# Kernel tuning notes

Hardware: AMD Instinct MI355X
Metric: run time of the kernel (lower is better)

## Reference

```python
import jax, jax.numpy as jnp
import numpy as np

N, E, F_IN, HID, K, CLS = 50000, 800000, 512, 128, 4, 40
EPS = 0.3


def setup_inputs() -> dict:
    key = jax.random.key(0)
    ks = jax.random.split(key, 6)
    x = jax.random.normal(ks[0], (N, F_IN), dtype=jnp.float32)
    edge_index = jax.random.randint(ks[1], (2, E), 0, N, dtype=jnp.int32)
    # xavier_normal with gain=1.414 ~ gain*sqrt(2/(fan_in+fan_out))
    t1_w = jax.random.normal(ks[2], (HID, F_IN), jnp.float32) * (1.414 * np.sqrt(2.0 / (F_IN + HID)))
    t1_b = jnp.zeros((HID,), jnp.float32)
    gate_w = jax.random.normal(ks[3], (K, 2 * HID), jnp.float32) * (1.414 * np.sqrt(2.0 / (2 * HID + 1)))
    gate_b = jnp.zeros((K,), jnp.float32)
    t2_w = jax.random.normal(ks[4], (CLS, HID), jnp.float32) * (1.414 * np.sqrt(2.0 / (HID + CLS)))
    t2_b = jnp.zeros((CLS,), jnp.float32)
    return dict(x=x, edge_index=edge_index, t1_w=t1_w, t1_b=t1_b,
                gate_w=gate_w, gate_b=gate_b, t2_w=t2_w, t2_b=t2_b)


def _fa_layer(h, row, col, nd, gw, gb):
    # gate(cat[h_row, h_col]) as two matvecs (equivalent to concat + Linear)
    d = h.shape[1]
    g = jnp.tanh(h[row] @ gw[:d] + h[col] @ gw[d:] + gb)   # [E]
    norm = g * nd[row] * nd[col]                           # [E]
    msg = norm[:, None] * h[row]                           # x_j = h[source], [E, HID]
    # aggregate (add) into target nodes
    return jax.ops.segment_sum(msg, col, num_segments=h.shape[0])


def reference(x, edge_index, t1_w, t1_b, gate_w, gate_b, t2_w, t2_b):
    row, col = edge_index[0], edge_index[1]
    deg = jax.ops.segment_sum(jnp.ones((E,), x.dtype), row, num_segments=N)
    nd = jnp.clip(deg, 1.0, None) ** -0.5                  # degree^{-1/2}, clamped at 1
    h = jax.nn.relu(x @ t1_w.T + t1_b)                     # [N, HID]
    raw = h
    for k in range(K):
        h = EPS * raw + _fa_layer(h, row, col, nd, gate_w[k], gate_b[k])
    return jax.nn.log_softmax(h @ t2_w.T + t2_b, axis=1)   # [N, CLS]
```

## Files before the change

kernel.cpp:

```cpp
#include <hip/hip_runtime.h>
#include <math.h>

#define N_NODES 50000
#define N_EDGES 800000
#define F_IN    512
#define HID     128
#define K_LAYERS 4
#define N_CLS   40
#define EPS_C   0.3f
#define CAP     64

#define GB_BLOCKS 782
#define PB_BLOCKS 1563

typedef __bf16 bf16x8 __attribute__((ext_vector_type(8)));
typedef float  f32x4  __attribute__((ext_vector_type(4)));
typedef float  f32x2  __attribute__((ext_vector_type(2)));

__device__ inline unsigned short bfb(float f) {
    __bf16 b = (__bf16)f;
    return __builtin_bit_cast(unsigned short, b);
}
__device__ inline unsigned pack2(float a, float b) {
    return (unsigned)bfb(a) | ((unsigned)bfb(b) << 16);
}
__device__ inline float lo2(unsigned v) { return __builtin_bit_cast(float, v << 16); }
__device__ inline float hi2(unsigned v) { return __builtin_bit_cast(float, v & 0xffff0000u); }
__device__ inline bf16x8 ld_frag(const unsigned short* p) {
    uint4 q = *(const uint4*)p;
    return __builtin_bit_cast(bf16x8, q);
}
__device__ inline void acc_fp8(float g, uint2 v, float* acc) {
    f32x2 p0 = __builtin_amdgcn_cvt_pk_f32_fp8((int)v.x, false);
    f32x2 p1 = __builtin_amdgcn_cvt_pk_f32_fp8((int)v.x, true);
    f32x2 p2 = __builtin_amdgcn_cvt_pk_f32_fp8((int)v.y, false);
    f32x2 p3 = __builtin_amdgcn_cvt_pk_f32_fp8((int)v.y, true);
    acc[0] = fmaf(g, p0[0], acc[0]); acc[1] = fmaf(g, p0[1], acc[1]);
    acc[2] = fmaf(g, p1[0], acc[2]); acc[3] = fmaf(g, p1[1], acc[3]);
    acc[4] = fmaf(g, p2[0], acc[4]); acc[5] = fmaf(g, p2[1], acc[5]);
    acc[6] = fmaf(g, p3[0], acc[6]); acc[7] = fmaf(g, p3[1], acc[7]);
}

__global__ __launch_bounds__(256) void k_prep(const int* __restrict__ row,
                                              const int* __restrict__ col,
                                              int* __restrict__ deg,
                                              int* __restrict__ cur,
                                              int* __restrict__ bucket) {
    int e0 = (blockIdx.x * 256 + threadIdx.x) * 2;
    if (e0 >= N_EDGES) return;
    int2 r2 = *(const int2*)&row[e0];
    int2 c2 = *(const int2*)&col[e0];
    atomicAdd(&deg[r2.x], 1);
    atomicAdd(&deg[r2.y], 1);
    int p0 = atomicAdd(&cur[c2.x], 1);
    int p1 = atomicAdd(&cur[c2.y], 1);
    if (p0 < CAP) bucket[((size_t)c2.x << 6) + p0] = r2.x;
    if (p1 < CAP) bucket[((size_t)c2.y << 6) + p1] = r2.y;
}

#define GS 72
__global__ __launch_bounds__(256) void k_gemm(const float* __restrict__ x,
                                              const float* __restrict__ w,
                                              const float* __restrict__ bias,
                                              const float* __restrict__ gw,
                                              const int* __restrict__ deg,
                                              unsigned* __restrict__ h0b,
                                              unsigned short* __restrict__ h08,
                                              float2* __restrict__ pn0,
                                              float* __restrict__ bn0) {
    __shared__ __attribute__((aligned(16))) unsigned short As[64 * GS];
    __shared__ __attribute__((aligned(16))) unsigned short Bs[128 * GS];
    __shared__ float redA[64];
    __shared__ float redB[64];
    const int t    = threadIdx.x;
    const int lane = t & 63;
    const int wv   = t >> 6;
    const int wrow = wv >> 1;
    const int wcol = wv & 1;
    const int nb0  = blockIdx.x * 64;
    const int m16  = lane & 15;
    const int quad = lane >> 4;

    if (t < 64) { redA[t] = 0.f; redB[t] = 0.f; }

    f32x4 acc[2][4];
#pragma unroll
    for (int mi = 0; mi < 2; mi++)
#pragma unroll
        for (int ni = 0; ni < 4; ni++) acc[mi][ni] = (f32x4){0.f, 0.f, 0.f, 0.f};

    for (int k0 = 0; k0 < F_IN; k0 += 64) {
        __syncthreads();
        {
            int r  = t & 63;
            int kh = (t >> 6) * 16;
            int n  = nb0 + r;
            unsigned short* pl = &As[r * GS + kh];
            if (n < N_NODES) {
                const float* px = &x[(size_t)n * F_IN + k0 + kh];
#pragma unroll
                for (int q = 0; q < 2; q++) {
                    float4 f0 = *(const float4*)(px + q * 8);
                    float4 f1 = *(const float4*)(px + q * 8 + 4);
                    *(ushort4*)(pl + q * 8)     = make_ushort4(bfb(f0.x), bfb(f0.y), bfb(f0.z), bfb(f0.w));
                    *(ushort4*)(pl + q * 8 + 4) = make_ushort4(bfb(f1.x), bfb(f1.y), bfb(f1.z), bfb(f1.w));
                }
            } else {
#pragma unroll
                for (int q = 0; q < 4; q++) *(ushort4*)(pl + q * 4) = make_ushort4(0, 0, 0, 0);
            }
        }
        {
            int j  = t & 127;
            int kh = (t >> 7) * 32;
            const float* pw = &w[(size_t)j * F_IN + k0 + kh];
            unsigned short* pl = &Bs[j * GS + kh];
#pragma unroll
            for (int q = 0; q < 4; q++) {
                float4 f0 = *(const float4*)(pw + q * 8);
                float4 f1 = *(const float4*)(pw + q * 8 + 4);
                *(ushort4*)(pl + q * 8)     = make_ushort4(bfb(f0.x), bfb(f0.y), bfb(f0.z), bfb(f0.w));
                *(ushort4*)(pl + q * 8 + 4) = make_ushort4(bfb(f1.x), bfb(f1.y), bfb(f1.z), bfb(f1.w));
            }
        }
        __syncthreads();
#pragma unroll
        for (int kk = 0; kk < 64; kk += 32) {
            bf16x8 af[2], bfr[4];
#pragma unroll
            for (int mi = 0; mi < 2; mi++)
                af[mi] = ld_frag(&As[(wrow * 32 + mi * 16 + m16) * GS + kk + quad * 8]);
#pragma unroll
            for (int ni = 0; ni < 4; ni++)
                bfr[ni] = ld_frag(&Bs[(wcol * 64 + ni * 16 + m16) * GS + kk + quad * 8]);
#pragma unroll
            for (int mi = 0; mi < 2; mi++)
#pragma unroll
                for (int ni = 0; ni < 4; ni++)
                    acc[mi][ni] = __builtin_amdgcn_mfma_f32_16x16x32_bf16(af[mi], bfr[ni], acc[mi][ni], 0, 0, 0);
        }
    }
    float bj[4], ga[4], gb2[4];
#pragma unroll
    for (int ni = 0; ni < 4; ni++) {
        int f = wcol * 64 + ni * 16 + m16;
        bj[ni]  = bias[f];
        ga[ni]  = gw[f];
        gb2[ni] = gw[128 + f];
    }
    unsigned short* h0u = (unsigned short*)h0b;
    unsigned char*  h8u = (unsigned char*)h08;
#pragma unroll
    for (int mi = 0; mi < 2; mi++)
#pragma unroll
        for (int reg = 0; reg < 4; reg++) {
            int loc = wrow * 32 + mi * 16 + quad * 4 + reg;
            int n   = nb0 + loc;
            float pa = 0.f, pb = 0.f;
            if (n < N_NODES) {
#pragma unroll
                for (int ni = 0; ni < 4; ni++) {
                    float v = fmaxf(acc[mi][ni][reg] + bj[ni], 0.f);
                    int f = wcol * 64 + ni * 16 + m16;
                    h0u[(size_t)n * HID + f] = bfb(v);
                    int pk = __builtin_amdgcn_cvt_pk_fp8_f32(v, v, 0, false);
                    h8u[(size_t)n * HID + f] = (unsigned char)(pk & 0xff);
                    pa = fmaf(v, ga[ni], pa);
                    pb = fmaf(v, gb2[ni], pb);
                }
            }
#pragma unroll
            for (int d = 1; d <= 8; d <<= 1) {
                pa += __shfl_xor(pa, d);
                pb += __shfl_xor(pb, d);
            }
            if (m16 == 0) {
                atomicAdd(&redA[loc], pa);
                atomicAdd(&redB[loc], pb);
            }
        }
    __syncthreads();
    if (t < 64) {
        int n = nb0 + t;
        if (n < N_NODES) {
            float dv = fmaxf((float)deg[n], 1.0f);
            pn0[n] = make_float2(redA[t], 1.0f / sqrtf(dv));
            bn0[n] = redB[t];
        }
    }
}

#define ISSUE_GRP(BASE, A, B, C, D)                                  \
    {                                                                \
        int ea = __shfl(idx, (BASE) + esub);                         \
        int eb = __shfl(idx, (BASE) + esub + 4);                     \
        int ec = __shfl(idx, (BASE) + esub + 8);                     \
        int ed = __shfl(idx, (BASE) + esub + 12);                    \
        A = h8v[(size_t)ea * 16 + fg];                               \
        B = h8v[(size_t)eb * 16 + fg];                               \
        C = h8v[(size_t)ec * 16 + fg];                               \
        D = h8v[(size_t)ed * 16 + fg];                               \
    }

__global__ __launch_bounds__(256) void k_agg7(const unsigned short* __restrict__ h8,
                                              const unsigned* __restrict__ h0b,
                                              const float2* __restrict__ pn,
                                              const float* __restrict__ bn,
                                              const int* __restrict__ bucket,
                                              const int* __restrict__ cur,
                                              const float* __restrict__ gb_all, int k,
                                              unsigned short* __restrict__ out8,
                                              unsigned* __restrict__ out16,
                                              const float* __restrict__ gwn,
                                              float2* __restrict__ pnn,
                                              float* __restrict__ bnn) {
    const int node = blockIdx.x * 4 + (threadIdx.x >> 6);
    const int lane = threadIdx.x & 63;
    if (node >= N_NODES) return;
    const int esub = lane >> 4;
    const int fg   = lane & 15;

    const int    cntr = cur[node];
    int          idx  = bucket[((size_t)node << 6) + lane];
    const float2 pno  = pn[node];
    const float  bwr  = bn[node];
    uint4 h0v = ((const uint4*)h0b)[(size_t)node * 16 + fg];

    const int   cnt = min(cntr, CAP);
    if (lane >= cnt) idx = 0;
    const float ndc = pno.y;
    const float bw  = bwr + gb_all[k];

    const uint2* h8v = (const uint2*)h8;
    uint2 v0 = make_uint2(0, 0), v1 = v0, v2 = v0, v3 = v0;
    uint2 w0 = v0, w1 = v0, w2 = v0, w3 = v0;
    if (cnt > 0)  ISSUE_GRP(0,  v0, v1, v2, v3);
    if (cnt > 16) ISSUE_GRP(16, w0, w1, w2, w3);

    float g = 0.f;
    if (lane < cnt) {
        float2 pr = pn[idx];
        float tt = pr.x + bw;
        float ex = __expf(tt + tt);
        g = (1.f - 2.f / (ex + 1.f)) * pr.y * ndc;
    }

    float acc[8];
#pragma unroll
    for (int j = 0; j < 8; j++) acc[j] = 0.f;

    for (int base = 0; base < cnt; base += 16) {
        float g0 = __shfl(g, base + esub);
        float g1 = __shfl(g, base + esub + 4);
        float g2 = __shfl(g, base + esub + 8);
        float g3 = __shfl(g, base + esub + 12);
        uint2 c0 = v0, c1 = v1, c2 = v2, c3 = v3;
        v0 = w0; v1 = w1; v2 = w2; v3 = w3;
        if (base + 32 < cnt) ISSUE_GRP(base + 32, w0, w1, w2, w3);
        acc_fp8(g0, c0, acc);
        acc_fp8(g1, c1, acc);
        acc_fp8(g2, c2, acc);
        acc_fp8(g3, c3, acc);
    }

#pragma unroll
    for (int j = 0; j < 8; j++) {
        acc[j] += __shfl_xor(acc[j], 16);
        acc[j] += __shfl_xor(acc[j], 32);
    }

    float of[8];
    of[0] = fmaf(EPS_C, lo2(h0v.x), acc[0]); of[1] = fmaf(EPS_C, hi2(h0v.x), acc[1]);
    of[2] = fmaf(EPS_C, lo2(h0v.y), acc[2]); of[3] = fmaf(EPS_C, hi2(h0v.y), acc[3]);
    of[4] = fmaf(EPS_C, lo2(h0v.z), acc[4]); of[5] = fmaf(EPS_C, hi2(h0v.z), acc[5]);
    of[6] = fmaf(EPS_C, lo2(h0v.w), acc[6]); of[7] = fmaf(EPS_C, hi2(h0v.w), acc[7]);
    if (esub == 0) {
        if (gwn) {
            int p0 = __builtin_amdgcn_cvt_pk_fp8_f32(of[0], of[1], 0, false);
            p0     = __builtin_amdgcn_cvt_pk_fp8_f32(of[2], of[3], p0, true);
            int p1 = __builtin_amdgcn_cvt_pk_fp8_f32(of[4], of[5], 0, false);
            p1     = __builtin_amdgcn_cvt_pk_fp8_f32(of[6], of[7], p1, true);
            ((uint2*)out8)[(size_t)node * 16 + fg] = make_uint2((unsigned)p0, (unsigned)p1);
        } else {
            uint4 ov;
            ov.x = pack2(of[0], of[1]); ov.y = pack2(of[2], of[3]);
            ov.z = pack2(of[4], of[5]); ov.w = pack2(of[6], of[7]);
            ((uint4*)out16)[(size_t)node * 16 + fg] = ov;
        }
    }

    if (gwn) {
        const float4* gw4 = (const float4*)gwn;
        float4 wa0 = gw4[fg * 2], wa1 = gw4[fg * 2 + 1];
        float4 wb0 = gw4[32 + fg * 2], wb1 = gw4[32 + fg * 2 + 1];
        float pa = of[0] * wa0.x + of[1] * wa0.y + of[2] * wa0.z + of[3] * wa0.w
                 + of[4] * wa1.x + of[5] * wa1.y + of[6] * wa1.z + of[7] * wa1.w;
        float pb = of[0] * wb0.x + of[1] * wb0.y + of[2] * wb0.z + of[3] * wb0.w
                 + of[4] * wb1.x + of[5] * wb1.y + of[6] * wb1.z + of[7] * wb1.w;
#pragma unroll
        for (int d = 1; d <= 8; d <<= 1) {
            pa += __shfl_xor(pa, d);
            pb += __shfl_xor(pb, d);
        }
        if (lane == 0) { pnn[node] = make_float2(pa, ndc); bnn[node] = pb; }
    }
}

#define OB_BLOCKS 3125
__global__ __launch_bounds__(256) void k_out(const unsigned* __restrict__ hb,
                                             const float* __restrict__ w2,
                                             const float* __restrict__ b2,
                                             float* __restrict__ out) {
    __shared__ float ws[N_CLS][HID + 1];
    __shared__ float hs[4][HID];
    __shared__ float bs[N_CLS];
    const int t = threadIdx.x;
    for (int i = t; i < N_CLS * HID; i += 256) {
        ws[i / HID][i % HID] = w2[i];
    }
    if (t < N_CLS) bs[t] = b2[t];
    __syncthreads();
    const int wv = t >> 6, lane = t & 63;
#pragma unroll
    for (int it = 0; it < 4; it++) {
        const int node = blockIdx.x * 16 + wv * 4 + it;
        unsigned v = hb[((size_t)node << 6) + lane];
        hs[wv][2 * lane]     = lo2(v);
        hs[wv][2 * lane + 1] = hi2(v);
        float z = -INFINITY;
        if (lane < N_CLS) {
            float s = bs[lane];
#pragma unroll 8
            for (int kk = 0; kk < HID; kk++) s = fmaf(hs[wv][kk], ws[lane][kk], s);
            z = s;
        }
        float mx = z;
#pragma unroll
        for (int d = 32; d > 0; d >>= 1) mx = fmaxf(mx, __shfl_xor(mx, d));
        float ex = (z == -INFINITY) ? 0.f : expf(z - mx);
        float sum = ex;
#pragma unroll
        for (int d = 32; d > 0; d >>= 1) sum += __shfl_xor(sum, d);
        if (lane < N_CLS)
            out[(size_t)node * N_CLS + lane] = z - mx - logf(sum);
    }
}

extern "C" void kernel_launch(void* const* d_in, const int* in_sizes, int n_in,
                              void* d_out, int out_size, void* d_ws, size_t ws_size,
                              hipStream_t stream) {
    const float* x   = (const float*)d_in[0];
    const int*   ei  = (const int*)d_in[1];
    const float* t1w = (const float*)d_in[2];
    const float* t1b = (const float*)d_in[3];
    const float* gw  = (const float*)d_in[4];
    const float* gb  = (const float*)d_in[5];
    const float* t2w = (const float*)d_in[6];
    const float* t2b = (const float*)d_in[7];
    float* out = (float*)d_out;

    const int* row = ei;
    const int* col = ei + N_EDGES;

    char* p = (char*)d_ws;
    auto alloc = [&](size_t bytes) -> char* {
        char* q = p;
        p += (bytes + 255) & ~(size_t)255;
        return q;
    };
    unsigned*       h0b  = (unsigned*)alloc(sizeof(unsigned) * (size_t)N_NODES * 64);
    unsigned*       hF   = (unsigned*)alloc(sizeof(unsigned) * (size_t)N_NODES * 64);
    unsigned short* h08  = (unsigned short*)alloc(sizeof(unsigned short) * (size_t)N_NODES * 64);
    unsigned short* hA8  = (unsigned short*)alloc(sizeof(unsigned short) * (size_t)N_NODES * 64);
    unsigned short* hB8  = (unsigned short*)alloc(sizeof(unsigned short) * (size_t)N_NODES * 64);
    float2*         pn0  = (float2*)alloc(sizeof(float2) * N_NODES);
    float2*         pn1  = (float2*)alloc(sizeof(float2) * N_NODES);
    float*          bn0  = (float*)alloc(sizeof(float) * N_NODES);
    float*          bn1  = (float*)alloc(sizeof(float) * N_NODES);
    int*            degi = (int*)alloc(sizeof(int) * N_NODES);
    int*            cur  = (int*)alloc(sizeof(int) * N_NODES);
    int*            bucket = (int*)alloc(sizeof(int) * (size_t)N_NODES * CAP);

    hipMemsetAsync(degi, 0, sizeof(int) * N_NODES, stream);
    hipMemsetAsync(cur,  0, sizeof(int) * N_NODES, stream);

    const int wb = (N_NODES + 3) / 4;

    k_prep<<<PB_BLOCKS, 256, 0, stream>>>(row, col, degi, cur, bucket);
    k_gemm<<<GB_BLOCKS, 256, 0, stream>>>(x, t1w, t1b, gw, degi, h0b, h08, pn0, bn0);

    const unsigned short* hc8 = h08;
    unsigned short* ring8[2] = {hA8, hB8};
    const float2* pc = pn0;  float2* pnx = pn1;
    const float*  bc = bn0;  float*  bnx = bn1;
    for (int k = 0; k < K_LAYERS; k++) {
        const float* gwn = (k + 1 < K_LAYERS) ? (gw + (size_t)(k + 1) * 2 * HID) : nullptr;
        unsigned short* hn8 = ring8[k & 1];
        k_agg7<<<wb, 256, 0, stream>>>(hc8, h0b, pc, bc, bucket, cur, gb, k,
                                       hn8, hF, gwn, pnx, bnx);
        hc8 = hn8;
        const float2* tp = pc; pc = pnx; pnx = (float2*)tp;
        const float*  tb = bc; bc = bnx; bnx = (float*)tb;
    }

    k_out<<<OB_BLOCKS, 256, 0, stream>>>(hF, t2w, t2b, out);
}
```

Before: 462.5 us.

## Split features into two planes and aggregate in two phases per layer

Node features are stored as two 64-column planes, and each aggregation layer runs as two launches, one per plane. This halves the random-gather working set each launch touches, so it has a better chance of staying cache-resident. The edge gate is computed once in the first phase and stored in a per-edge buffer for the second phase. The prep kernel is fused into the GEMM launch, the GEMM tile grows to 128 rows, and nontemporal loads and stores are used. The cost is twice the aggregation launches, extra gate-buffer traffic, and a read-modify-write of the next layer's projections.

```diff
diff --git a/kernel.cpp b/kernel.cpp
--- a/kernel.cpp
+++ b/kernel.cpp
@@ -10,12 +10,15 @@
 #define EPS_C   0.3f
 #define CAP     64
 
-#define GB_BLOCKS 782
+#define GB_BLOCKS 391
 #define PB_BLOCKS 1563
+#define PS0 ((size_t)N_NODES * 64)
 
 typedef __bf16 bf16x8 __attribute__((ext_vector_type(8)));
 typedef float  f32x4  __attribute__((ext_vector_type(4)));
 typedef float  f32x2  __attribute__((ext_vector_type(2)));
+typedef unsigned u32x2 __attribute__((ext_vector_type(2)));
+typedef unsigned u32x4 __attribute__((ext_vector_type(4)));
 
 __device__ inline unsigned short bfb(float f) {
     __bf16 b = (__bf16)f;
@@ -41,65 +44,67 @@
     acc[6] = fmaf(g, p3[0], acc[6]); acc[7] = fmaf(g, p3[1], acc[7]);
 }
 
-__global__ __launch_bounds__(256) void k_prep(const int* __restrict__ row,
-                                              const int* __restrict__ col,
-                                              int* __restrict__ deg,
-                                              int* __restrict__ cur,
-                                              int* __restrict__ bucket) {
-    int e0 = (blockIdx.x * 256 + threadIdx.x) * 2;
-    if (e0 >= N_EDGES) return;
-    int2 r2 = *(const int2*)&row[e0];
-    int2 c2 = *(const int2*)&col[e0];
-    atomicAdd(&deg[r2.x], 1);
-    atomicAdd(&deg[r2.y], 1);
-    int p0 = atomicAdd(&cur[c2.x], 1);
-    int p1 = atomicAdd(&cur[c2.y], 1);
-    if (p0 < CAP) bucket[((size_t)c2.x << 6) + p0] = r2.x;
-    if (p1 < CAP) bucket[((size_t)c2.y << 6) + p1] = r2.y;
-}
-
 #define GS 72
-__global__ __launch_bounds__(256) void k_gemm(const float* __restrict__ x,
-                                              const float* __restrict__ w,
-                                              const float* __restrict__ bias,
-                                              const float* __restrict__ gw,
-                                              const int* __restrict__ deg,
-                                              unsigned* __restrict__ h0b,
-                                              unsigned short* __restrict__ h08,
-                                              float2* __restrict__ pn0,
-                                              float* __restrict__ bn0) {
-    __shared__ __attribute__((aligned(16))) unsigned short As[64 * GS];
+__global__ __launch_bounds__(256) void k_gemm_prep(const float* __restrict__ x,
+                                                   const float* __restrict__ w,
+                                                   const float* __restrict__ bias,
+                                                   const float* __restrict__ gw,
+                                                   const int* __restrict__ row,
+                                                   const int* __restrict__ col,
+                                                   int* __restrict__ deg,
+                                                   int* __restrict__ cur,
+                                                   int* __restrict__ bucket,
+                                                   unsigned short* __restrict__ h0,
+                                                   unsigned char* __restrict__ h8,
+                                                   float2* __restrict__ pn0,
+                                                   float* __restrict__ bn0) {
+    if (blockIdx.x >= GB_BLOCKS) {
+        int e0 = (blockIdx.x - GB_BLOCKS) * 512 + threadIdx.x * 2;
+        if (e0 < N_EDGES) {
+            int2 r2 = *(const int2*)&row[e0];
+            int2 c2 = *(const int2*)&col[e0];
+            atomicAdd(&deg[r2.x], 1);
+            atomicAdd(&deg[r2.y], 1);
+            int p0 = atomicAdd(&cur[c2.x], 1);
+            int p1 = atomicAdd(&cur[c2.y], 1);
+            if (p0 < CAP) bucket[((size_t)c2.x << 6) + p0] = r2.x;
+            if (p1 < CAP) bucket[((size_t)c2.y << 6) + p1] = r2.y;
+        }
+        return;
+    }
+
+    __shared__ __attribute__((aligned(16))) unsigned short As[128 * GS];
     __shared__ __attribute__((aligned(16))) unsigned short Bs[128 * GS];
-    __shared__ float redA[64];
-    __shared__ float redB[64];
+    __shared__ float redA[128];
+    __shared__ float redB[128];
     const int t    = threadIdx.x;
     const int lane = t & 63;
     const int wv   = t >> 6;
     const int wrow = wv >> 1;
     const int wcol = wv & 1;
-    const int nb0  = blockIdx.x * 64;
+    const int nb0  = blockIdx.x * 128;
     const int m16  = lane & 15;
     const int quad = lane >> 4;
 
-    if (t < 64) { redA[t] = 0.f; redB[t] = 0.f; }
-
-    f32x4 acc[2][4];
-#pragma unroll
-    for (int mi = 0; mi < 2; mi++)
+    if (t < 128) { redA[t] = 0.f; redB[t] = 0.f; }
+
+    f32x4 acc[4][4];
+#pragma unroll
+    for (int mi = 0; mi < 4; mi++)
 #pragma unroll
         for (int ni = 0; ni < 4; ni++) acc[mi][ni] = (f32x4){0.f, 0.f, 0.f, 0.f};
 
     for (int k0 = 0; k0 < F_IN; k0 += 64) {
         __syncthreads();
         {
-            int r  = t & 63;
-            int kh = (t >> 6) * 16;
+            int r  = t & 127;
+            int kh = (t >> 7) * 32;
             int n  = nb0 + r;
             unsigned short* pl = &As[r * GS + kh];
             if (n < N_NODES) {
                 const float* px = &x[(size_t)n * F_IN + k0 + kh];
 #pragma unroll
-                for (int q = 0; q < 2; q++) {
+                for (int q = 0; q < 4; q++) {
                     float4 f0 = *(const float4*)(px + q * 8);
                     float4 f1 = *(const float4*)(px + q * 8 + 4);
                     *(ushort4*)(pl + q * 8)     = make_ushort4(bfb(f0.x), bfb(f0.y), bfb(f0.z), bfb(f0.w));
@@ -107,7 +112,7 @@
                 }
             } else {
 #pragma unroll
-                for (int q = 0; q < 4; q++) *(ushort4*)(pl + q * 4) = make_ushort4(0, 0, 0, 0);
+                for (int q = 0; q < 8; q++) *(ushort4*)(pl + q * 4) = make_ushort4(0, 0, 0, 0);
             }
         }
         {
@@ -126,15 +131,15 @@
         __syncthreads();
 #pragma unroll
         for (int kk = 0; kk < 64; kk += 32) {
-            bf16x8 af[2], bfr[4];
-#pragma unroll
-            for (int mi = 0; mi < 2; mi++)
-                af[mi] = ld_frag(&As[(wrow * 32 + mi * 16 + m16) * GS + kk + quad * 8]);
+            bf16x8 af[4], bfr[4];
+#pragma unroll
+            for (int mi = 0; mi < 4; mi++)
+                af[mi] = ld_frag(&As[(wrow * 64 + mi * 16 + m16) * GS + kk + quad * 8]);
 #pragma unroll
             for (int ni = 0; ni < 4; ni++)
                 bfr[ni] = ld_frag(&Bs[(wcol * 64 + ni * 16 + m16) * GS + kk + quad * 8]);
 #pragma unroll
-            for (int mi = 0; mi < 2; mi++)
+            for (int mi = 0; mi < 4; mi++)
 #pragma unroll
                 for (int ni = 0; ni < 4; ni++)
                     acc[mi][ni] = __builtin_amdgcn_mfma_f32_16x16x32_bf16(af[mi], bfr[ni], acc[mi][ni], 0, 0, 0);
@@ -148,23 +153,23 @@
         ga[ni]  = gw[f];
         gb2[ni] = gw[128 + f];
     }
-    unsigned short* h0u = (unsigned short*)h0b;
-    unsigned char*  h8u = (unsigned char*)h08;
-#pragma unroll
-    for (int mi = 0; mi < 2; mi++)
+    unsigned short* h0pl = h0 + (size_t)wcol * PS0;
+    unsigned char*  h8pl = h8 + (size_t)wcol * PS0;
+#pragma unroll
+    for (int mi = 0; mi < 4; mi++)
 #pragma unroll
         for (int reg = 0; reg < 4; reg++) {
-            int loc = wrow * 32 + mi * 16 + quad * 4 + reg;
+            int loc = wrow * 64 + mi * 16 + quad * 4 + reg;
             int n   = nb0 + loc;
             float pa = 0.f, pb = 0.f;
             if (n < N_NODES) {
 #pragma unroll
                 for (int ni = 0; ni < 4; ni++) {
                     float v = fmaxf(acc[mi][ni][reg] + bj[ni], 0.f);
-                    int f = wcol * 64 + ni * 16 + m16;
-                    h0u[(size_t)n * HID + f] = bfb(v);
+                    int f16 = ni * 16 + m16;
+                    h0pl[(size_t)n * 64 + f16] = bfb(v);
                     int pk = __builtin_amdgcn_cvt_pk_fp8_f32(v, v, 0, false);
-                    h8u[(size_t)n * HID + f] = (unsigned char)(pk & 0xff);
+                    h8pl[(size_t)n * 64 + f16] = (unsigned char)(pk & 0xff);
                     pa = fmaf(v, ga[ni], pa);
                     pb = fmaf(v, gb2[ni], pb);
                 }
@@ -180,134 +185,139 @@
             }
         }
     __syncthreads();
-    if (t < 64) {
+    if (t < 128) {
         int n = nb0 + t;
         if (n < N_NODES) {
-            float dv = fmaxf((float)deg[n], 1.0f);
-            pn0[n] = make_float2(redA[t], 1.0f / sqrtf(dv));
+            ((float*)pn0)[2 * (size_t)n] = redA[t];
             bn0[n] = redB[t];
         }
     }
 }
 
-#define ISSUE_GRP(BASE, A, B, C, D)                                  \
-    {                                                                \
-        int ea = __shfl(idx, (BASE) + esub);                         \
-        int eb = __shfl(idx, (BASE) + esub + 4);                     \
-        int ec = __shfl(idx, (BASE) + esub + 8);                     \
-        int ed = __shfl(idx, (BASE) + esub + 12);                    \
-        A = h8v[(size_t)ea * 16 + fg];                               \
-        B = h8v[(size_t)eb * 16 + fg];                               \
-        C = h8v[(size_t)ec * 16 + fg];                               \
-        D = h8v[(size_t)ed * 16 + fg];                               \
-    }
-
-__global__ __launch_bounds__(256) void k_agg7(const unsigned short* __restrict__ h8,
-                                              const unsigned* __restrict__ h0b,
+__global__ __launch_bounds__(256) void k_nd(const int* __restrict__ deg,
+                                            float2* __restrict__ pn0) {
+    int n = blockIdx.x * 256 + threadIdx.x;
+    if (n < N_NODES) {
+        float dv = fmaxf((float)deg[n], 1.0f);
+        ((float*)pn0)[2 * (size_t)n + 1] = 1.0f / sqrtf(dv);
+    }
+}
+
+__global__ __launch_bounds__(256) void k_aggp(const unsigned char* __restrict__ h8p,
+                                              const unsigned short* __restrict__ h0p,
                                               const float2* __restrict__ pn,
                                               const float* __restrict__ bn,
                                               const int* __restrict__ bucket,
                                               const int* __restrict__ cur,
-                                              const float* __restrict__ gb_all, int k,
-                                              unsigned short* __restrict__ out8,
-                                              unsigned* __restrict__ out16,
+                                              const float* __restrict__ gb_all, int k, int phase,
+                                              float* __restrict__ garr,
+                                              unsigned char* __restrict__ out8p,
+                                              unsigned short* __restrict__ out16p,
                                               const float* __restrict__ gwn,
                                               float2* __restrict__ pnn,
                                               float* __restrict__ bnn) {
     const int node = blockIdx.x * 4 + (threadIdx.x >> 6);
     const int lane = threadIdx.x & 63;
     if (node >= N_NODES) return;
-    const int esub = lane >> 4;
-    const int fg   = lane & 15;
-
-    const int    cntr = cur[node];
-    int          idx  = bucket[((size_t)node << 6) + lane];
-    const float2 pno  = pn[node];
-    const float  bwr  = bn[node];
-    uint4 h0v = ((const uint4*)h0b)[(size_t)node * 16 + fg];
-
-    const int   cnt = min(cntr, CAP);
+    const int esub = lane >> 3;
+    const int fgrp = lane & 7;
+
+    const int cntr = cur[node];
+    int idx = __builtin_nontemporal_load(&bucket[((size_t)node << 6) + lane]);
+    u32x4 h0v = __builtin_nontemporal_load((const u32x4*)(h0p + ((size_t)node << 6)) + fgrp);
+    const int cnt = min(cntr, CAP);
     if (lane >= cnt) idx = 0;
-    const float ndc = pno.y;
-    const float bw  = bwr + gb_all[k];
-
-    const uint2* h8v = (const uint2*)h8;
-    uint2 v0 = make_uint2(0, 0), v1 = v0, v2 = v0, v3 = v0;
-    uint2 w0 = v0, w1 = v0, w2 = v0, w3 = v0;
-    if (cnt > 0)  ISSUE_GRP(0,  v0, v1, v2, v3);
-    if (cnt > 16) ISSUE_GRP(16, w0, w1, w2, w3);
 
     float g = 0.f;
-    if (lane < cnt) {
-        float2 pr = pn[idx];
-        float tt = pr.x + bw;
-        float ex = __expf(tt + tt);
-        g = (1.f - 2.f / (ex + 1.f)) * pr.y * ndc;
-    }
+    float ndc = 0.f;
+    if (phase == 0) {
+        const float2 pno = pn[node];
+        const float  bw  = bn[node] + gb_all[k];
+        ndc = pno.y;
+        if (lane < cnt) {
+            float2 pr = pn[idx];
+            float tt = pr.x + bw;
+            float ex = __expf(tt + tt);
+            g = (1.f - 2.f / (ex + 1.f)) * pr.y * ndc;
+        }
+        if (lane < cnt) garr[((size_t)node << 6) + lane] = g;
+    } else {
+        if (lane < cnt) g = garr[((size_t)node << 6) + lane];
+    }
+
+    const uint2* h8v = (const uint2*)h8p;
+    uint2 va = make_uint2(0, 0), vb = va;
+    if (cnt > 0) { int e = __shfl(idx, esub);     va = h8v[(size_t)e * 8 + fgrp]; }
+    if (cnt > 8) { int e = __shfl(idx, 8 + esub); vb = h8v[(size_t)e * 8 + fgrp]; }
 
     float acc[8];
 #pragma unroll
     for (int j = 0; j < 8; j++) acc[j] = 0.f;
 
-    for (int base = 0; base < cnt; base += 16) {
-        float g0 = __shfl(g, base + esub);
-        float g1 = __shfl(g, base + esub + 4);
-        float g2 = __shfl(g, base + esub + 8);
-        float g3 = __shfl(g, base + esub + 12);
-        uint2 c0 = v0, c1 = v1, c2 = v2, c3 = v3;
-        v0 = w0; v1 = w1; v2 = w2; v3 = w3;
-        if (base + 32 < cnt) ISSUE_GRP(base + 32, w0, w1, w2, w3);
-        acc_fp8(g0, c0, acc);
-        acc_fp8(g1, c1, acc);
-        acc_fp8(g2, c2, acc);
-        acc_fp8(g3, c3, acc);
+    for (int base = 0; base < cnt; base += 8) {
+        float gg = __shfl(g, base + esub);
+        uint2 cv = va;
+        va = vb;
+        if (base + 16 < cnt) { int e = __shfl(idx, base + 16 + esub); vb = h8v[(size_t)e * 8 + fgrp]; }
+        acc_fp8(gg, cv, acc);
     }
 
 #pragma unroll
     for (int j = 0; j < 8; j++) {
+        acc[j] += __shfl_xor(acc[j], 8);
         acc[j] += __shfl_xor(acc[j], 16);
         acc[j] += __shfl_xor(acc[j], 32);
     }
 
     float of[8];
-    of[0] = fmaf(EPS_C, lo2(h0v.x), acc[0]); of[1] = fmaf(EPS_C, hi2(h0v.x), acc[1]);
-    of[2] = fmaf(EPS_C, lo2(h0v.y), acc[2]); of[3] = fmaf(EPS_C, hi2(h0v.y), acc[3]);
-    of[4] = fmaf(EPS_C, lo2(h0v.z), acc[4]); of[5] = fmaf(EPS_C, hi2(h0v.z), acc[5]);
-    of[6] = fmaf(EPS_C, lo2(h0v.w), acc[6]); of[7] = fmaf(EPS_C, hi2(h0v.w), acc[7]);
+    of[0] = fmaf(EPS_C, lo2(h0v[0]), acc[0]); of[1] = fmaf(EPS_C, hi2(h0v[0]), acc[1]);
+    of[2] = fmaf(EPS_C, lo2(h0v[1]), acc[2]); of[3] = fmaf(EPS_C, hi2(h0v[1]), acc[3]);
+    of[4] = fmaf(EPS_C, lo2(h0v[2]), acc[4]); of[5] = fmaf(EPS_C, hi2(h0v[2]), acc[5]);
+    of[6] = fmaf(EPS_C, lo2(h0v[3]), acc[6]); of[7] = fmaf(EPS_C, hi2(h0v[3]), acc[7]);
     if (esub == 0) {
         if (gwn) {
             int p0 = __builtin_amdgcn_cvt_pk_fp8_f32(of[0], of[1], 0, false);
             p0     = __builtin_amdgcn_cvt_pk_fp8_f32(of[2], of[3], p0, true);
             int p1 = __builtin_amdgcn_cvt_pk_fp8_f32(of[4], of[5], 0, false);
             p1     = __builtin_amdgcn_cvt_pk_fp8_f32(of[6], of[7], p1, true);
-            ((uint2*)out8)[(size_t)node * 16 + fg] = make_uint2((unsigned)p0, (unsigned)p1);
+            u32x2 ov; ov[0] = (unsigned)p0; ov[1] = (unsigned)p1;
+            __builtin_nontemporal_store(ov, (u32x2*)(out8p + ((size_t)node << 6)) + fgrp);
         } else {
-            uint4 ov;
-            ov.x = pack2(of[0], of[1]); ov.y = pack2(of[2], of[3]);
-            ov.z = pack2(of[4], of[5]); ov.w = pack2(of[6], of[7]);
-            ((uint4*)out16)[(size_t)node * 16 + fg] = ov;
+            u32x4 ov;
+            ov[0] = pack2(of[0], of[1]); ov[1] = pack2(of[2], of[3]);
+            ov[2] = pack2(of[4], of[5]); ov[3] = pack2(of[6], of[7]);
+            __builtin_nontemporal_store(ov, (u32x4*)(out16p + ((size_t)node << 6)) + fgrp);
         }
     }
 
     if (gwn) {
         const float4* gw4 = (const float4*)gwn;
-        float4 wa0 = gw4[fg * 2], wa1 = gw4[fg * 2 + 1];
-        float4 wb0 = gw4[32 + fg * 2], wb1 = gw4[32 + fg * 2 + 1];
+        int bo = (phase << 4) + (fgrp << 1);
+        float4 wa0 = gw4[bo], wa1 = gw4[bo + 1];
+        float4 wb0 = gw4[32 + bo], wb1 = gw4[32 + bo + 1];
         float pa = of[0] * wa0.x + of[1] * wa0.y + of[2] * wa0.z + of[3] * wa0.w
                  + of[4] * wa1.x + of[5] * wa1.y + of[6] * wa1.z + of[7] * wa1.w;
         float pb = of[0] * wb0.x + of[1] * wb0.y + of[2] * wb0.z + of[3] * wb0.w
                  + of[4] * wb1.x + of[5] * wb1.y + of[6] * wb1.z + of[7] * wb1.w;
 #pragma unroll
-        for (int d = 1; d <= 8; d <<= 1) {
+        for (int d = 1; d <= 4; d <<= 1) {
             pa += __shfl_xor(pa, d);
             pb += __shfl_xor(pb, d);
         }
-        if (lane == 0) { pnn[node] = make_float2(pa, ndc); bnn[node] = pb; }
+        if (lane == 0) {
+            if (phase == 0) {
+                pnn[node] = make_float2(pa, ndc);
+                bnn[node] = pb;
+            } else {
+                float2 tacc = pnn[node]; tacc.x += pa; pnn[node] = tacc;
+                bnn[node] += pb;
+            }
+        }
     }
 }
 
 #define OB_BLOCKS 3125
-__global__ __launch_bounds__(256) void k_out(const unsigned* __restrict__ hb,
+__global__ __launch_bounds__(256) void k_out(const unsigned short* __restrict__ hFp,
                                              const float* __restrict__ w2,
                                              const float* __restrict__ b2,
                                              float* __restrict__ out) {
@@ -324,7 +334,9 @@
 #pragma unroll
     for (int it = 0; it < 4; it++) {
         const int node = blockIdx.x * 16 + wv * 4 + it;
-        unsigned v = hb[((size_t)node << 6) + lane];
+        unsigned v;
+        if (lane < 32) v = ((const unsigned*)hFp)[(size_t)node * 32 + lane];
+        else           v = ((const unsigned*)(hFp + PS0))[(size_t)node * 32 + lane - 32];
         hs[wv][2 * lane]     = lo2(v);
         hs[wv][2 * lane + 1] = hi2(v);
         float z = -INFINITY;
@@ -368,11 +380,12 @@
         p += (bytes + 255) & ~(size_t)255;
         return q;
     };
-    unsigned*       h0b  = (unsigned*)alloc(sizeof(unsigned) * (size_t)N_NODES * 64);
-    unsigned*       hF   = (unsigned*)alloc(sizeof(unsigned) * (size_t)N_NODES * 64);
-    unsigned short* h08  = (unsigned short*)alloc(sizeof(unsigned short) * (size_t)N_NODES * 64);
-    unsigned short* hA8  = (unsigned short*)alloc(sizeof(unsigned short) * (size_t)N_NODES * 64);
-    unsigned short* hB8  = (unsigned short*)alloc(sizeof(unsigned short) * (size_t)N_NODES * 64);
+    unsigned short* h0   = (unsigned short*)alloc(2 * PS0 * 2);
+    unsigned short* hF   = (unsigned short*)alloc(2 * PS0 * 2);
+    unsigned char*  h08  = (unsigned char*)alloc(2 * PS0);
+    unsigned char*  hA8  = (unsigned char*)alloc(2 * PS0);
+    unsigned char*  hB8  = (unsigned char*)alloc(2 * PS0);
+    float*          garr = (float*)alloc(sizeof(float) * (size_t)N_NODES * CAP);
     float2*         pn0  = (float2*)alloc(sizeof(float2) * N_NODES);
     float2*         pn1  = (float2*)alloc(sizeof(float2) * N_NODES);
     float*          bn0  = (float*)alloc(sizeof(float) * N_NODES);
@@ -386,18 +399,27 @@
 
     const int wb = (N_NODES + 3) / 4;
 
-    k_prep<<<PB_BLOCKS, 256, 0, stream>>>(row, col, degi, cur, bucket);
-    k_gemm<<<GB_BLOCKS, 256, 0, stream>>>(x, t1w, t1b, gw, degi, h0b, h08, pn0, bn0);
-
-    const unsigned short* hc8 = h08;
-    unsigned short* ring8[2] = {hA8, hB8};
+    k_gemm_prep<<<GB_BLOCKS + PB_BLOCKS, 256, 0, stream>>>(x, t1w, t1b, gw,
+                                                           row, col, degi, cur, bucket,
+                                                           h0, h08, pn0, bn0);
+    k_nd<<<(N_NODES + 255) / 256, 256, 0, stream>>>(degi, pn0);
+
+    const unsigned char* hc8 = h08;
+    unsigned char* ring8[2] = {hA8, hB8};
     const float2* pc = pn0;  float2* pnx = pn1;
     const float*  bc = bn0;  float*  bnx = bn1;
     for (int k = 0; k < K_LAYERS; k++) {
         const float* gwn = (k + 1 < K_LAYERS) ? (gw + (size_t)(k + 1) * 2 * HID) : nullptr;
-        unsigned short* hn8 = ring8[k & 1];
-        k_agg7<<<wb, 256, 0, stream>>>(hc8, h0b, pc, bc, bucket, cur, gb, k,
-                                       hn8, hF, gwn, pnx, bnx);
+        unsigned char* hn8 = ring8[k & 1];
+        for (int phase = 0; phase < 2; phase++) {
+            k_aggp<<<wb, 256, 0, stream>>>(hc8 + phase * PS0,
+                                           h0 + phase * PS0,
+                                           pc, bc, bucket, cur, gb, k, phase,
+                                           garr,
+                                           hn8 + phase * PS0,
+                                           hF + phase * PS0,
+                                           gwn, pnx, bnx);
+        }
         hc8 = hn8;
         const float2* tp = pc; pc = pnx; pnx = (float2*)tp;
         const float*  tb = bc; bc = bnx; bnx = (float*)tb;
```

After: 481.8 us. 1.04x slower.
